# Kernel optimization log

Hardware: AMD Instinct MI355X
Metric: run time of the kernel (lower is better)

Reference implementation:

```python
import jax, jax.numpy as jnp
import numpy as np

N = 16384
F_IN = 256
F_OUT = 256


def setup_inputs() -> dict:
    key = jax.random.key(0)
    k1, k2, k3 = jax.random.split(key, 3)
    x = jax.random.normal(k1, (N, F_IN), dtype=jnp.float32)
    # dense 0/1 adjacency (original masks with adj[j] == 1)
    adj = jax.random.randint(k2, (N, N), 0, 2, dtype=jnp.int32)
    # glorot-uniform init for weight [2F_in, F_out]
    stdv = np.sqrt(6.0 / (2 * F_IN + F_OUT)).astype(np.float32)
    weight = jax.random.uniform(k3, (2 * F_IN, F_OUT), dtype=jnp.float32,
                                minval=-stdv, maxval=stdv)
    bias = jnp.zeros((F_OUT,), dtype=jnp.float32)
    return {"x": x, "adj": adj, "weight": weight, "bias": bias}


def reference(x, adj, weight, bias):
    # Mean over neighbors (adj row == 1): segment-mean expressed as a
    # normalized dense matmul -- equivalent to the per-row boolean-mask mean.
    a = adj.astype(x.dtype)                      # [N, N]
    deg = jnp.sum(a, axis=1, keepdims=True)      # [N, 1]
    x1 = (a @ x) / deg                           # [N, F] neighbor mean
    n_x = jnp.concatenate([x1, x], axis=1)       # [N, 2F]
    return n_x @ weight + bias                   # [N, F_out]
```

## Files before the change

### kernel.cpp

```cpp
#include <hip/hip_runtime.h>
#include <hip/hip_bf16.h>
#include <stdint.h>


typedef short bf16x8 __attribute__((ext_vector_type(8)));
typedef float f32x4  __attribute__((ext_vector_type(4)));

__device__ __forceinline__ uint32_t pack_bf16_rne(float lo, float hi) {
    uint32_t ul = __float_as_uint(lo);
    uint32_t uh = __float_as_uint(hi);
    ul = (ul + 0x7fffu + ((ul >> 16) & 1u)) >> 16;
    uh = (uh + 0x7fffu + ((uh >> 16) & 1u)) >> 16;
    return ul | (uh << 16);
}

__global__ __launch_bounds__(256) void k_transpose_w(const float* __restrict__ w,
                                                     uint16_t* __restrict__ wt) {
    int idx = blockIdx.x * 256 + threadIdx.x;
    int n = idx >> 8;
    int k = idx & 255;
    int row = (n < 256) ? k : (256 + k);
    int col = (n < 256) ? n : (n - 256);
    uint32_t u = __float_as_uint(w[row * 256 + col]);
    u = (u + 0x7fffu + ((u >> 16) & 1u)) >> 16;
    wt[idx] = (uint16_t)u;
}

__global__ __launch_bounds__(256) void k_small_gemm(const float* __restrict__ x,
                                                    const uint16_t* __restrict__ wt,
                                                    const float* __restrict__ bias,
                                                    uint16_t* __restrict__ yTt,
                                                    float* __restrict__ z) {
    __shared__ uint16_t As[128 * 32];
    __shared__ uint16_t Bs[128 * 32];

    const int t  = threadIdx.x;
    const int ct = blockIdx.x;
    const int rt = blockIdx.y;
    const int m0 = rt * 128;
    const int n0 = ct * 128;

    const int lane = t & 63, w = t >> 6;
    const int wr = w >> 1, wc = w & 1;
    const int l15 = lane & 15, quad = lane >> 4;

    f32x4 acc[4][4] = {};

    float4 a_reg[4];
    uint4  b_reg[2];

#pragma unroll
    for (int i = 0; i < 4; ++i) {
        int f4 = t + 256 * i, row = f4 >> 3, c4 = f4 & 7;
        a_reg[i] = *(const float4*)(x + (m0 + row) * 256 + c4 * 4);
    }
#pragma unroll
    for (int i = 0; i < 2; ++i) {
        int u4 = t + 256 * i, n_l = u4 >> 2, part = u4 & 3;
        b_reg[i] = *(const uint4*)(wt + (n0 + n_l) * 256 + part * 8);
    }

    for (int kk = 0; kk < 8; ++kk) {
        __syncthreads();
#pragma unroll
        for (int i = 0; i < 4; ++i) {
            int f4 = t + 256 * i, row = f4 >> 3, c4 = f4 & 7;
            uint2 p;
            p.x = pack_bf16_rne(a_reg[i].x, a_reg[i].y);
            p.y = pack_bf16_rne(a_reg[i].z, a_reg[i].w);
            *(uint2*)(As + row * 32 + c4 * 4) = p;
        }
#pragma unroll
        for (int i = 0; i < 2; ++i) {
            int u4 = t + 256 * i, n_l = u4 >> 2, part = u4 & 3;
            *(uint4*)(Bs + n_l * 32 + part * 8) = b_reg[i];
        }
        if (kk < 7) {
            int k0 = (kk + 1) * 32;
#pragma unroll
            for (int i = 0; i < 4; ++i) {
                int f4 = t + 256 * i, row = f4 >> 3, c4 = f4 & 7;
                a_reg[i] = *(const float4*)(x + (m0 + row) * 256 + k0 + c4 * 4);
            }
#pragma unroll
            for (int i = 0; i < 2; ++i) {
                int u4 = t + 256 * i, n_l = u4 >> 2, part = u4 & 3;
                b_reg[i] = *(const uint4*)(wt + (n0 + n_l) * 256 + k0 + part * 8);
            }
        }
        __syncthreads();

        bf16x8 a_frag[4], b_frag[4];
#pragma unroll
        for (int fr = 0; fr < 4; ++fr)
            a_frag[fr] = *(const bf16x8*)(As + (wr * 64 + fr * 16 + l15) * 32 + quad * 8);
#pragma unroll
        for (int fc = 0; fc < 4; ++fc)
            b_frag[fc] = *(const bf16x8*)(Bs + (wc * 64 + fc * 16 + l15) * 32 + quad * 8);
#pragma unroll
        for (int fr = 0; fr < 4; ++fr)
#pragma unroll
            for (int fc = 0; fc < 4; ++fc)
                acc[fr][fc] = __builtin_amdgcn_mfma_f32_16x16x32_bf16(
                    a_frag[fr], b_frag[fc], acc[fr][fc], 0, 0, 0);
    }

    if (ct < 2) {
#pragma unroll
        for (int fr = 0; fr < 4; ++fr) {
            int m_base = m0 + wr * 64 + fr * 16 + quad * 4;
#pragma unroll
            for (int fc = 0; fc < 4; ++fc) {
                int n_g = n0 + wc * 64 + fc * 16 + l15;
                uint2 pp;
                pp.x = pack_bf16_rne(acc[fr][fc][0], acc[fr][fc][1]);
                pp.y = pack_bf16_rne(acc[fr][fc][2], acc[fr][fc][3]);
                *(uint2*)(yTt + (size_t)(m_base >> 5) * 8192 + n_g * 32 + (m_base & 31)) = pp;
            }
        }
    } else {
#pragma unroll
        for (int fr = 0; fr < 4; ++fr) {
            int m_base = m0 + wr * 64 + fr * 16 + quad * 4;
#pragma unroll
            for (int fc = 0; fc < 4; ++fc) {
                int n_g = (n0 - 256) + wc * 64 + fc * 16 + l15;
                float bv = bias[n_g];
#pragma unroll
                for (int r = 0; r < 4; ++r)
                    z[(size_t)(m_base + r) * 256 + n_g] = acc[fr][fc][r] + bv;
            }
        }
    }
}

#define A_STRIDE 36
#define B_STRIDE 36
#define A_SZ (64 * A_STRIDE)
#define B_SZ (256 * B_STRIDE)
#define KITER 256

#define STEP(ARD, BRD, AWR, BWR, KK)                                            \
  do {                                                                          \
    if ((KK) < KITER - 2) {                                   \
      bN0 = *(const uint4*)(pB);                                                \
      bN1 = *(const uint4*)(pB + 4096);                                         \
      pB += 8192;                                                               \
    }                                                                           \
    if ((KK) < KITER - 3) {                                   \
      aN = pa4[0]; pa4 += 8;                                                    \
    }                                                                           \
    if ((KK) < KITER - 1) {                              \
      degp += aQ0.x + aQ0.y + aQ0.z + aQ0.w;                                    \
      uint2 pv;                                                                 \
      pv.x = (uint32_t)(aQ0.x | (aQ0.y << 16)) * 0x3F80u;                       \
      pv.y = (uint32_t)(aQ0.z | (aQ0.w << 16)) * 0x3F80u;                       \
      *(uint2*)&As##AWR[a_lds] = pv;                                            \
      *(uint4*)&Bs##BWR[b_lds0] = bC0;                                          \
      *(uint4*)&Bs##BWR[b_lds1] = bC1;                                          \
    }                                                                           \
    {                                                                           \
      bf16x8 af[2], bfr[4];                                                     \
      _Pragma("unroll") for (int fr = 0; fr < 2; ++fr) {                        \
        int row = wr * 32 + fr * 16 + l15;                                      \
        af[fr] = *(const bf16x8*)(As##ARD + row * A_STRIDE + quad * 8);         \
      }                                                                         \
      _Pragma("unroll") for (int fc = 0; fc < 4; ++fc) {                        \
        int n = wc * 64 + fc * 16 + l15;                                        \
        bfr[fc] = *(const bf16x8*)(Bs##BRD + n * B_STRIDE + quad * 8);          \
      }                                                                         \
      _Pragma("unroll") for (int fr = 0; fr < 2; ++fr)                          \
        _Pragma("unroll") for (int fc = 0; fc < 4; ++fc)                        \
          acc[fr][fc] = __builtin_amdgcn_mfma_f32_16x16x32_bf16(                \
              af[fr], bfr[fc], acc[fr][fc], 0, 0, 0);                           \
    }                                                                           \
    aQ0 = aQ1; aQ1 = aQ2; aQ2 = aN;                                             \
    bC0 = bN0; bC1 = bN1;                                                       \
    asm volatile("s_waitcnt lgkmcnt(0)\n\ts_barrier" ::: "memory");             \
  } while (0)

__global__ __launch_bounds__(512, 4) void k_big_gemm(const int* __restrict__ adj,
                                                     const uint16_t* __restrict__ yTt,
                                                     float* __restrict__ part,
                                                     int* __restrict__ degw) {
    __shared__ uint16_t As0[A_SZ], As1[A_SZ], As2[A_SZ];
    __shared__ uint16_t Bs0[B_SZ], Bs1[B_SZ], Bs2[B_SZ];

    const int t = threadIdx.x;
    const int m0 = blockIdx.x * 64;
    const int ky = blockIdx.y;
    const int lane = t & 63, w = t >> 6;
    const int wr = w >> 2, wc = w & 3;
    const int l15 = lane & 15, quad = lane >> 4;

    f32x4 acc[2][4] = {};

    const int a_n = t >> 3, a_c4 = t & 7;
    const int4* pa4 = (const int4*)(adj + (size_t)(m0 + a_n) * 16384 + ky * 8192) + a_c4;
    const int a_lds = a_n * A_STRIDE + a_c4 * 4;

    const uint16_t* pB = yTt + (size_t)(ky * 256) * 8192 + t * 8;
    const int b_s0 = t, b_s1 = t + 512;
    const int b_lds0 = (b_s0 >> 2) * B_STRIDE + (b_s0 & 3) * 8;
    const int b_lds1 = (b_s1 >> 2) * B_STRIDE + (b_s1 & 3) * 8;

    int4 a0 = pa4[0];
    int4 aQ0 = pa4[8];
    int4 aQ1 = pa4[16];
    int4 aQ2;
    int4 aN = aQ1;
    pa4 += 24;
    uint4 b00 = *(const uint4*)(pB);
    uint4 b01 = *(const uint4*)(pB + 4096);
    pB += 8192;
    uint4 bC0 = *(const uint4*)(pB);
    uint4 bC1 = *(const uint4*)(pB + 4096);
    pB += 8192;
    uint4 bN0 = bC0, bN1 = bC1;

    int degp = a0.x + a0.y + a0.z + a0.w;
    {
        uint2 pv;
        pv.x = (uint32_t)(a0.x | (a0.y << 16)) * 0x3F80u;
        pv.y = (uint32_t)(a0.z | (a0.w << 16)) * 0x3F80u;
        *(uint2*)&As0[a_lds] = pv;
        *(uint4*)&Bs0[b_lds0] = b00;
        *(uint4*)&Bs0[b_lds1] = b01;
    }
    asm volatile("s_waitcnt lgkmcnt(0)\n\ts_barrier" ::: "memory");

    for (int kk = 0; kk < KITER - 4; kk += 3) {
        STEP(0, 0, 1, 1, kk);
        STEP(1, 1, 2, 2, kk + 1);
        STEP(2, 2, 0, 0, kk + 2);
    }
    STEP(0, 0, 1, 1, 252);
    STEP(1, 1, 2, 2, 253);
    STEP(2, 2, 0, 0, 254);
    STEP(0, 0, 1, 1, 255);

    degp += __shfl_down(degp, 4);
    degp += __shfl_down(degp, 2);
    degp += __shfl_down(degp, 1);
    if ((t & 7) == 0) degw[ky * 16384 + m0 + a_n] = degp;

    float* pc = part + (size_t)ky * 16384 * 256;
#pragma unroll
    for (int fr = 0; fr < 2; ++fr) {
#pragma unroll
        for (int r = 0; r < 4; ++r) {
            int m_l = wr * 32 + fr * 16 + quad * 4 + r;
            size_t mrow = (size_t)(m0 + m_l) * 256;
#pragma unroll
            for (int fc = 0; fc < 4; ++fc) {
                int n_g = wc * 64 + fc * 16 + l15;
                pc[mrow + n_g] = acc[fr][fc][r];
            }
        }
    }
}

__global__ __launch_bounds__(256) void k_reduce(const float* __restrict__ part,
                                                const int* __restrict__ degw,
                                                const float* __restrict__ z,
                                                float* __restrict__ out) {
    int i4 = blockIdx.x * 256 + threadIdx.x;
    int m = i4 >> 6;
    float4 p0 = ((const float4*)part)[i4];
    float4 p1 = ((const float4*)part)[i4 + 16384 * 64];
    float4 zz = ((const float4*)z)[i4];
    float inv = 1.0f / (float)(degw[m] + degw[16384 + m]);
    float4 o;
    o.x = (p0.x + p1.x) * inv + zz.x;
    o.y = (p0.y + p1.y) * inv + zz.y;
    o.z = (p0.z + p1.z) * inv + zz.z;
    o.w = (p0.w + p1.w) * inv + zz.w;
    ((float4*)out)[i4] = o;
}

extern "C" void kernel_launch(void* const* d_in, const int* in_sizes, int n_in,
                              void* d_out, int out_size, void* d_ws, size_t ws_size,
                              hipStream_t stream) {
    const float* x      = (const float*)d_in[0];
    const int*   adj    = (const int*)d_in[1];
    const float* weight = (const float*)d_in[2];
    const float* bias   = (const float*)d_in[3];
    float* out = (float*)d_out;

    char* wsb = (char*)d_ws;
    uint16_t* wt   = (uint16_t*)(wsb);
    uint16_t* yTt  = (uint16_t*)(wsb + 262144);
    float*    z    = (float*)(wsb + 262144 + 8388608);
    float*    partb= (float*)(wsb + 262144 + 8388608 + 16777216);
    int*      degw = (int*)(wsb + 262144 + 8388608 + 16777216 + 33554432);

    k_transpose_w<<<512, 256, 0, stream>>>(weight, wt);
    k_small_gemm<<<dim3(4, 128), 256, 0, stream>>>(x, wt, bias, yTt, z);
    k_big_gemm<<<dim3(256, 2), 512, 0, stream>>>(adj, yTt, partb, degw);
    k_reduce<<<4096, 256, 0, stream>>>(partb, degw, z, out);
}
```

Before: 1.426 ms.

## Enlarge big GEMM tile to 128 rows with K=64 double-buffered register prefetch

Rewrites the adjacency GEMM kernel to use 128-row M tiles and 64-wide K steps, with each thread loading four int4 of adj and four uint4 of B per step. Global loads are issued two stages ahead into register sets and synchronised with explicit vmcnt waits, LDS goes from triple to double buffering, and MFMA sections run at raised wave priority. The larger tile halves how often each block re-reads B and doubles the MFMA work per barrier, at the cost of more registers and only 256 blocks, which means lower occupancy on the MI355X.

Result: slower. 1.664 ms (+16.7%).

```diff
diff --git a/kernel.cpp b/kernel.cpp
--- a/kernel.cpp
+++ b/kernel.cpp
@@ -134,123 +134,132 @@
     }
 }
 
-#define A_STRIDE 36
-#define B_STRIDE 36
-#define A_SZ (64 * A_STRIDE)
-#define B_SZ (256 * B_STRIDE)
-#define KITER 256
-
-#define STEP(ARD, BRD, AWR, BWR, KK)                                            \
-  do {                                                                          \
-    if ((KK) < KITER - 2) {                                   \
-      bN0 = *(const uint4*)(pB);                                                \
-      bN1 = *(const uint4*)(pB + 4096);                                         \
-      pB += 8192;                                                               \
-    }                                                                           \
-    if ((KK) < KITER - 3) {                                   \
-      aN = pa4[0]; pa4 += 8;                                                    \
-    }                                                                           \
-    if ((KK) < KITER - 1) {                              \
-      degp += aQ0.x + aQ0.y + aQ0.z + aQ0.w;                                    \
-      uint2 pv;                                                                 \
-      pv.x = (uint32_t)(aQ0.x | (aQ0.y << 16)) * 0x3F80u;                       \
-      pv.y = (uint32_t)(aQ0.z | (aQ0.w << 16)) * 0x3F80u;                       \
-      *(uint2*)&As##AWR[a_lds] = pv;                                            \
-      *(uint4*)&Bs##BWR[b_lds0] = bC0;                                          \
-      *(uint4*)&Bs##BWR[b_lds1] = bC1;                                          \
-    }                                                                           \
-    {                                                                           \
-      bf16x8 af[2], bfr[4];                                                     \
-      _Pragma("unroll") for (int fr = 0; fr < 2; ++fr) {                        \
-        int row = wr * 32 + fr * 16 + l15;                                      \
-        af[fr] = *(const bf16x8*)(As##ARD + row * A_STRIDE + quad * 8);         \
-      }                                                                         \
-      _Pragma("unroll") for (int fc = 0; fc < 4; ++fc) {                        \
-        int n = wc * 64 + fc * 16 + l15;                                        \
-        bfr[fc] = *(const bf16x8*)(Bs##BRD + n * B_STRIDE + quad * 8);          \
-      }                                                                         \
-      _Pragma("unroll") for (int fr = 0; fr < 2; ++fr)                          \
-        _Pragma("unroll") for (int fc = 0; fc < 4; ++fc)                        \
-          acc[fr][fc] = __builtin_amdgcn_mfma_f32_16x16x32_bf16(                \
-              af[fr], bfr[fc], acc[fr][fc], 0, 0, 0);                           \
-    }                                                                           \
-    aQ0 = aQ1; aQ1 = aQ2; aQ2 = aN;                                             \
-    bC0 = bN0; bC1 = bN1;                                                       \
-    asm volatile("s_waitcnt lgkmcnt(0)\n\ts_barrier" ::: "memory");             \
+#define BM 128
+#define NT 128
+#define A_ST 72
+#define B_ST 72
+
+#define ISSUE(SET, STEP_)                                                     \
+  do {                                                                        \
+    const int4*  ap_ = pa4 + (size_t)(STEP_) * 16;                            \
+    const uint4* bp_ = pb4 + (size_t)(STEP_) * 2048;                          \
+    aR[SET][0] = ap_[0]; aR[SET][1] = ap_[1];                                 \
+    aR[SET][2] = ap_[2]; aR[SET][3] = ap_[3];                                 \
+    bR[SET][0] = bp_[0]; bR[SET][1] = bp_[1];                                 \
+    bR[SET][2] = bp_[2]; bR[SET][3] = bp_[3];                                 \
   } while (0)
 
-__global__ __launch_bounds__(512, 4) void k_big_gemm(const int* __restrict__ adj,
-                                                     const uint16_t* __restrict__ yTt,
-                                                     float* __restrict__ part,
-                                                     int* __restrict__ degw) {
-    __shared__ uint16_t As0[A_SZ], As1[A_SZ], As2[A_SZ];
-    __shared__ uint16_t Bs0[B_SZ], Bs1[B_SZ], Bs2[B_SZ];
+#define STAGE(SET, BUF)                                                       \
+  do {                                                                        \
+    degp += aR[SET][0].x + aR[SET][0].y + aR[SET][0].z + aR[SET][0].w         \
+          + aR[SET][1].x + aR[SET][1].y + aR[SET][1].z + aR[SET][1].w         \
+          + aR[SET][2].x + aR[SET][2].y + aR[SET][2].z + aR[SET][2].w         \
+          + aR[SET][3].x + aR[SET][3].y + aR[SET][3].z + aR[SET][3].w;        \
+    uint4 w0_, w1_;                                                           \
+    w0_.x = (uint32_t)(aR[SET][0].x | (aR[SET][0].y << 16)) * 0x3F80u;        \
+    w0_.y = (uint32_t)(aR[SET][0].z | (aR[SET][0].w << 16)) * 0x3F80u;        \
+    w0_.z = (uint32_t)(aR[SET][1].x | (aR[SET][1].y << 16)) * 0x3F80u;        \
+    w0_.w = (uint32_t)(aR[SET][1].z | (aR[SET][1].w << 16)) * 0x3F80u;        \
+    w1_.x = (uint32_t)(aR[SET][2].x | (aR[SET][2].y << 16)) * 0x3F80u;        \
+    w1_.y = (uint32_t)(aR[SET][2].z | (aR[SET][2].w << 16)) * 0x3F80u;        \
+    w1_.z = (uint32_t)(aR[SET][3].x | (aR[SET][3].y << 16)) * 0x3F80u;        \
+    w1_.w = (uint32_t)(aR[SET][3].z | (aR[SET][3].w << 16)) * 0x3F80u;        \
+    *(uint4*)&As[BUF][a_wr]      = w0_;                                       \
+    *(uint4*)&As[BUF][a_wr + 8]  = w1_;                                       \
+    *(uint4*)&Bs[BUF][b_wr]      = bR[SET][0];                                \
+    *(uint4*)&Bs[BUF][b_wr + 8]  = bR[SET][1];                                \
+    *(uint4*)&Bs[BUF][b_wr + 16] = bR[SET][2];                                \
+    *(uint4*)&Bs[BUF][b_wr + 24] = bR[SET][3];                                \
+  } while (0)
+
+#define COMPUTE(BUF)                                                          \
+  do {                                                                        \
+    _Pragma("unroll") for (int kh = 0; kh < 2; ++kh) {                        \
+      bf16x8 af[4], bfr[4];                                                   \
+      _Pragma("unroll") for (int fr = 0; fr < 4; ++fr)                        \
+        af[fr] = *(const bf16x8*)&As[BUF][(wr * 64 + fr * 16 + l15) * A_ST +  \
+                                          kh * 32 + quad * 8];                \
+      _Pragma("unroll") for (int fc = 0; fc < 4; ++fc)                        \
+        bfr[fc] = *(const bf16x8*)&Bs[BUF][(wc * 64 + fc * 16 + l15) * B_ST + \
+                                           kh * 32 + quad * 8];               \
+      _Pragma("unroll") for (int fr = 0; fr < 4; ++fr)                        \
+        _Pragma("unroll") for (int fc = 0; fc < 4; ++fc)                      \
+          acc[fr][fc] = __builtin_amdgcn_mfma_f32_16x16x32_bf16(              \
+              af[fr], bfr[fc], acc[fr][fc], 0, 0, 0);                         \
+    }                                                                         \
+  } while (0)
+
+__global__ __launch_bounds__(512) void k_big_gemm(const int* __restrict__ adj,
+                                                  const uint16_t* __restrict__ yTt,
+                                                  float* __restrict__ part,
+                                                  int* __restrict__ degw) {
+    __shared__ __align__(16) uint16_t As[2][BM * A_ST];
+    __shared__ __align__(16) uint16_t Bs[2][256 * B_ST];
 
     const int t = threadIdx.x;
-    const int m0 = blockIdx.x * 64;
+    const int m0 = blockIdx.x * BM;
     const int ky = blockIdx.y;
     const int lane = t & 63, w = t >> 6;
     const int wr = w >> 2, wc = w & 3;
     const int l15 = lane & 15, quad = lane >> 4;
 
-    f32x4 acc[2][4] = {};
-
-    const int a_n = t >> 3, a_c4 = t & 7;
-    const int4* pa4 = (const int4*)(adj + (size_t)(m0 + a_n) * 16384 + ky * 8192) + a_c4;
-    const int a_lds = a_n * A_STRIDE + a_c4 * 4;
-
-    const uint16_t* pB = yTt + (size_t)(ky * 256) * 8192 + t * 8;
-    const int b_s0 = t, b_s1 = t + 512;
-    const int b_lds0 = (b_s0 >> 2) * B_STRIDE + (b_s0 & 3) * 8;
-    const int b_lds1 = (b_s1 >> 2) * B_STRIDE + (b_s1 & 3) * 8;
-
-    int4 a0 = pa4[0];
-    int4 aQ0 = pa4[8];
-    int4 aQ1 = pa4[16];
-    int4 aQ2;
-    int4 aN = aQ1;
-    pa4 += 24;
-    uint4 b00 = *(const uint4*)(pB);
-    uint4 b01 = *(const uint4*)(pB + 4096);
-    pB += 8192;
-    uint4 bC0 = *(const uint4*)(pB);
-    uint4 bC1 = *(const uint4*)(pB + 4096);
-    pB += 8192;
-    uint4 bN0 = bC0, bN1 = bC1;
-
-    int degp = a0.x + a0.y + a0.z + a0.w;
-    {
-        uint2 pv;
-        pv.x = (uint32_t)(a0.x | (a0.y << 16)) * 0x3F80u;
-        pv.y = (uint32_t)(a0.z | (a0.w << 16)) * 0x3F80u;
-        *(uint2*)&As0[a_lds] = pv;
-        *(uint4*)&Bs0[b_lds0] = b00;
-        *(uint4*)&Bs0[b_lds1] = b01;
-    }
+    f32x4 acc[4][4] = {};
+
+    const int a_row = t >> 2, a_c = t & 3;
+    const int4* pa4 = (const int4*)(adj + (size_t)(m0 + a_row) * 16384 + ky * 8192) + a_c * 4;
+    const int a_wr = a_row * A_ST + a_c * 16;
+
+    const int b_kt = t >> 8, b_n = t & 255;
+    const uint4* pb4 = (const uint4*)(yTt + ((size_t)ky * 256 + b_kt) * 8192 + b_n * 32);
+    const int b_wr = b_n * B_ST + b_kt * 32;
+
+    int4  aR[2][4];
+    uint4 bR[2][4];
+    int degp = 0;
+
+    ISSUE(0, 0);
+    asm volatile("" ::: "memory");
+    ISSUE(1, 1);
+    asm volatile("s_waitcnt vmcnt(8)" ::: "memory");
+    STAGE(0, 0);
     asm volatile("s_waitcnt lgkmcnt(0)\n\ts_barrier" ::: "memory");
 
-    for (int kk = 0; kk < KITER - 4; kk += 3) {
-        STEP(0, 0, 1, 1, kk);
-        STEP(1, 1, 2, 2, kk + 1);
-        STEP(2, 2, 0, 0, kk + 2);
-    }
-    STEP(0, 0, 1, 1, 252);
-    STEP(1, 1, 2, 2, 253);
-    STEP(2, 2, 0, 0, 254);
-    STEP(0, 0, 1, 1, 255);
-
-    degp += __shfl_down(degp, 4);
+    for (int tt = 0; tt < NT - 2; tt += 2) {
+        ISSUE(0, tt + 2);
+        asm volatile("s_waitcnt vmcnt(8)" ::: "memory");
+        STAGE(1, 1);
+        __builtin_amdgcn_s_setprio(1);
+        COMPUTE(0);
+        __builtin_amdgcn_s_setprio(0);
+        asm volatile("s_waitcnt lgkmcnt(0)\n\ts_barrier" ::: "memory");
+
+        ISSUE(1, tt + 3);
+        asm volatile("s_waitcnt vmcnt(8)" ::: "memory");
+        STAGE(0, 0);
+        __builtin_amdgcn_s_setprio(1);
+        COMPUTE(1);
+        __builtin_amdgcn_s_setprio(0);
+        asm volatile("s_waitcnt lgkmcnt(0)\n\ts_barrier" ::: "memory");
+    }
+    asm volatile("s_waitcnt vmcnt(0)" ::: "memory");
+    STAGE(1, 1);
+    __builtin_amdgcn_s_setprio(1);
+    COMPUTE(0);
+    __builtin_amdgcn_s_setprio(0);
+    asm volatile("s_waitcnt lgkmcnt(0)\n\ts_barrier" ::: "memory");
+    COMPUTE(1);
+
     degp += __shfl_down(degp, 2);
     degp += __shfl_down(degp, 1);
-    if ((t & 7) == 0) degw[ky * 16384 + m0 + a_n] = degp;
-
-    float* pc = part + (size_t)ky * 16384 * 256;
-#pragma unroll
-    for (int fr = 0; fr < 2; ++fr) {
+    if ((t & 3) == 0) degw[ky * 16384 + m0 + a_row] = degp;
+
+    float* pc = part + (size_t)ky * 16384 * 256 + (size_t)m0 * 256;
+#pragma unroll
+    for (int fr = 0; fr < 4; ++fr) {
 #pragma unroll
         for (int r = 0; r < 4; ++r) {
-            int m_l = wr * 32 + fr * 16 + quad * 4 + r;
-            size_t mrow = (size_t)(m0 + m_l) * 256;
+            int m_l = wr * 64 + fr * 16 + quad * 4 + r;
+            size_t mrow = (size_t)m_l * 256;
 #pragma unroll
             for (int fc = 0; fc < 4; ++fc) {
                 int n_g = wc * 64 + fc * 16 + l15;
@@ -296,6 +305,6 @@
 
     k_transpose_w<<<512, 256, 0, stream>>>(weight, wt);
     k_small_gemm<<<dim3(4, 128), 256, 0, stream>>>(x, wt, bias, yTt, z);
-    k_big_gemm<<<dim3(256, 2), 512, 0, stream>>>(adj, yTt, partb, degw);
+    k_big_gemm<<<dim3(128, 2), 512, 0, stream>>>(adj, yTt, partb, degw);
     k_reduce<<<4096, 256, 0, stream>>>(partb, degw, z, out);
 }
```

## Load B fragments directly from global into registers and remap blocks per XCD

Applied to the files above, without the earlier changes.

Removes the LDS staging for the B operand (the transposed y matrix). Each wave now loads its MFMA B fragments straight from global memory into registers, prefetched one step ahead, which drops the LDS writes and reads and shrinks shared memory to the A buffers only. The block index is also remapped so that blocks with the same K-half and neighbouring M tiles land on the same XCD, aiming for better L2 reuse of adjacency rows and B. In exchange, B tiles that were shared through LDS are now fetched redundantly by each wave row, raising global/L2 traffic and register pressure.

Result: slower. 1.494 ms (+4.8%).

```diff
diff --git a/kernel.cpp b/kernel.cpp
--- a/kernel.cpp
+++ b/kernel.cpp
@@ -135,47 +135,39 @@
 }
 
 #define A_STRIDE 36
-#define B_STRIDE 36
 #define A_SZ (64 * A_STRIDE)
-#define B_SZ (256 * B_STRIDE)
 #define KITER 256
 
-#define STEP(ARD, BRD, AWR, BWR, KK)                                            \
+#define STEP(ARD, AWR, KK)                                                      \
   do {                                                                          \
-    if ((KK) < KITER - 2) {                                   \
-      bN0 = *(const uint4*)(pB);                                                \
-      bN1 = *(const uint4*)(pB + 4096);                                         \
+    if ((KK) < KITER - 1) {                                \
+      _Pragma("unroll") for (int fc = 0; fc < 4; ++fc)                          \
+        bN[fc] = *(const bf16x8*)(pB + fc * 512);                               \
       pB += 8192;                                                               \
     }                                                                           \
     if ((KK) < KITER - 3) {                                   \
       aN = pa4[0]; pa4 += 8;                                                    \
     }                                                                           \
-    if ((KK) < KITER - 1) {                              \
+    if ((KK) < KITER - 1) {                           \
       degp += aQ0.x + aQ0.y + aQ0.z + aQ0.w;                                    \
       uint2 pv;                                                                 \
       pv.x = (uint32_t)(aQ0.x | (aQ0.y << 16)) * 0x3F80u;                       \
       pv.y = (uint32_t)(aQ0.z | (aQ0.w << 16)) * 0x3F80u;                       \
       *(uint2*)&As##AWR[a_lds] = pv;                                            \
-      *(uint4*)&Bs##BWR[b_lds0] = bC0;                                          \
-      *(uint4*)&Bs##BWR[b_lds1] = bC1;                                          \
     }                                                                           \
     {                                                                           \
-      bf16x8 af[2], bfr[4];                                                     \
+      bf16x8 af[2];                                                             \
       _Pragma("unroll") for (int fr = 0; fr < 2; ++fr) {                        \
         int row = wr * 32 + fr * 16 + l15;                                      \
         af[fr] = *(const bf16x8*)(As##ARD + row * A_STRIDE + quad * 8);         \
       }                                                                         \
-      _Pragma("unroll") for (int fc = 0; fc < 4; ++fc) {                        \
-        int n = wc * 64 + fc * 16 + l15;                                        \
-        bfr[fc] = *(const bf16x8*)(Bs##BRD + n * B_STRIDE + quad * 8);          \
-      }                                                                         \
       _Pragma("unroll") for (int fr = 0; fr < 2; ++fr)                          \
         _Pragma("unroll") for (int fc = 0; fc < 4; ++fc)                        \
           acc[fr][fc] = __builtin_amdgcn_mfma_f32_16x16x32_bf16(                \
-              af[fr], bfr[fc], acc[fr][fc], 0, 0, 0);                           \
+              af[fr], bC[fc], acc[fr][fc], 0, 0, 0);                            \
     }                                                                           \
     aQ0 = aQ1; aQ1 = aQ2; aQ2 = aN;                                             \
-    bC0 = bN0; bC1 = bN1;                                                       \
+    _Pragma("unroll") for (int fc = 0; fc < 4; ++fc) bC[fc] = bN[fc];           \
     asm volatile("s_waitcnt lgkmcnt(0)\n\ts_barrier" ::: "memory");             \
   } while (0)
 
@@ -184,11 +176,12 @@
                                                      float* __restrict__ part,
                                                      int* __restrict__ degw) {
     __shared__ uint16_t As0[A_SZ], As1[A_SZ], As2[A_SZ];
-    __shared__ uint16_t Bs0[B_SZ], Bs1[B_SZ], Bs2[B_SZ];
 
     const int t = threadIdx.x;
-    const int m0 = blockIdx.x * 64;
-    const int ky = blockIdx.y;
+    const int id   = blockIdx.x + (int)gridDim.x * blockIdx.y;
+    const int xcd  = id & 7, slot = id >> 3;
+    const int ky   = xcd >> 2;
+    const int m0   = ((xcd & 3) * 64 + slot) * 64;
     const int lane = t & 63, w = t >> 6;
     const int wr = w >> 2, wc = w & 3;
     const int l15 = lane & 15, quad = lane >> 4;
@@ -199,45 +192,43 @@
     const int4* pa4 = (const int4*)(adj + (size_t)(m0 + a_n) * 16384 + ky * 8192) + a_c4;
     const int a_lds = a_n * A_STRIDE + a_c4 * 4;
 
-    const uint16_t* pB = yTt + (size_t)(ky * 256) * 8192 + t * 8;
-    const int b_s0 = t, b_s1 = t + 512;
-    const int b_lds0 = (b_s0 >> 2) * B_STRIDE + (b_s0 & 3) * 8;
-    const int b_lds1 = (b_s1 >> 2) * B_STRIDE + (b_s1 & 3) * 8;
+    const uint16_t* pB = yTt + (size_t)(ky * 256) * 8192
+                       + (size_t)(wc * 64 + l15) * 32 + quad * 8;
+
+    bf16x8 bC[4], bN[4];
+    int4 aQ0, aQ1, aQ2, aN;
+    int degp;
 
     int4 a0 = pa4[0];
-    int4 aQ0 = pa4[8];
-    int4 aQ1 = pa4[16];
-    int4 aQ2;
-    int4 aN = aQ1;
+    aQ0 = pa4[8];
+    aQ1 = pa4[16];
+    aQ2 = aQ1;
+    aN  = aQ1;
     pa4 += 24;
-    uint4 b00 = *(const uint4*)(pB);
-    uint4 b01 = *(const uint4*)(pB + 4096);
+#pragma unroll
+    for (int fc = 0; fc < 4; ++fc) bN[fc] = *(const bf16x8*)(pB + fc * 512);
     pB += 8192;
-    uint4 bC0 = *(const uint4*)(pB);
-    uint4 bC1 = *(const uint4*)(pB + 4096);
-    pB += 8192;
-    uint4 bN0 = bC0, bN1 = bC1;
-
-    int degp = a0.x + a0.y + a0.z + a0.w;
+#pragma unroll
+    for (int fc = 0; fc < 4; ++fc) bC[fc] = bN[fc];
+
+    degp = a0.x + a0.y + a0.z + a0.w;
     {
         uint2 pv;
         pv.x = (uint32_t)(a0.x | (a0.y << 16)) * 0x3F80u;
         pv.y = (uint32_t)(a0.z | (a0.w << 16)) * 0x3F80u;
         *(uint2*)&As0[a_lds] = pv;
-        *(uint4*)&Bs0[b_lds0] = b00;
-        *(uint4*)&Bs0[b_lds1] = b01;
     }
     asm volatile("s_waitcnt lgkmcnt(0)\n\ts_barrier" ::: "memory");
 
     for (int kk = 0; kk < KITER - 4; kk += 3) {
-        STEP(0, 0, 1, 1, kk);
-        STEP(1, 1, 2, 2, kk + 1);
-        STEP(2, 2, 0, 0, kk + 2);
-    }
-    STEP(0, 0, 1, 1, 252);
-    STEP(1, 1, 2, 2, 253);
-    STEP(2, 2, 0, 0, 254);
-    STEP(0, 0, 1, 1, 255);
+        STEP(0, 1, kk);
+        STEP(1, 2, kk + 1);
+        STEP(2, 0, kk + 2);
+    }
+    STEP(0, 1, 252);
+    STEP(1, 2, 253);
+    STEP(2, 0, 254);
+    STEP(0, 1, 255);
 
     degp += __shfl_down(degp, 4);
     degp += __shfl_down(degp, 2);
```

## Deepen adjacency prefetch, use nontemporal loads/stores, remap blocks across XCDs

Applied to the files above, without the earlier changes.

Reads the streamed adjacency matrix with nontemporal loads and deepens its register prefetch queue from three to four stages to hide more global latency. Writes partial results with nontemporal stores so they do not pollute cache. Remaps the flat block id so that each XCD handles one K-half and a contiguous row range, so the shared B operand (yTt) stays local to each XCD's L2. Costs extra registers for the deeper queue, which could hurt occupancy at 512 threads with 4 blocks per CU.

New measurement: 1.425 ms. No clear change (-0.0%).

```diff
diff --git a/kernel.cpp b/kernel.cpp
--- a/kernel.cpp
+++ b/kernel.cpp
@@ -5,6 +5,7 @@
 
 typedef short bf16x8 __attribute__((ext_vector_type(8)));
 typedef float f32x4  __attribute__((ext_vector_type(4)));
+typedef int   i32x4  __attribute__((ext_vector_type(4)));
 
 __device__ __forceinline__ uint32_t pack_bf16_rne(float lo, float hi) {
     uint32_t ul = __float_as_uint(lo);
@@ -147,14 +148,14 @@
       bN1 = *(const uint4*)(pB + 4096);                                         \
       pB += 8192;                                                               \
     }                                                                           \
-    if ((KK) < KITER - 3) {                                   \
-      aN = pa4[0]; pa4 += 8;                                                    \
+    if ((KK) < KITER - 4) {                     \
+      aN = __builtin_nontemporal_load(pa4); pa4 += 8;                           \
     }                                                                           \
     if ((KK) < KITER - 1) {                              \
-      degp += aQ0.x + aQ0.y + aQ0.z + aQ0.w;                                    \
+      degp += q1.x + q1.y + q1.z + q1.w;                                        \
       uint2 pv;                                                                 \
-      pv.x = (uint32_t)(aQ0.x | (aQ0.y << 16)) * 0x3F80u;                       \
-      pv.y = (uint32_t)(aQ0.z | (aQ0.w << 16)) * 0x3F80u;                       \
+      pv.x = (uint32_t)(q1.x | (q1.y << 16)) * 0x3F80u;                         \
+      pv.y = (uint32_t)(q1.z | (q1.w << 16)) * 0x3F80u;                         \
       *(uint2*)&As##AWR[a_lds] = pv;                                            \
       *(uint4*)&Bs##BWR[b_lds0] = bC0;                                          \
       *(uint4*)&Bs##BWR[b_lds1] = bC1;                                          \
@@ -174,7 +175,7 @@
           acc[fr][fc] = __builtin_amdgcn_mfma_f32_16x16x32_bf16(                \
               af[fr], bfr[fc], acc[fr][fc], 0, 0, 0);                           \
     }                                                                           \
-    aQ0 = aQ1; aQ1 = aQ2; aQ2 = aN;                                             \
+    q1 = q2; q2 = q3; q3 = aN;                                                  \
     bC0 = bN0; bC1 = bN1;                                                       \
     asm volatile("s_waitcnt lgkmcnt(0)\n\ts_barrier" ::: "memory");             \
   } while (0)
@@ -187,8 +188,10 @@
     __shared__ uint16_t Bs0[B_SZ], Bs1[B_SZ], Bs2[B_SZ];
 
     const int t = threadIdx.x;
-    const int m0 = blockIdx.x * 64;
-    const int ky = blockIdx.y;
+    const int id   = blockIdx.x + (int)gridDim.x * blockIdx.y;
+    const int xcd  = id & 7, slot = id >> 3;
+    const int ky   = xcd >> 2;
+    const int m0   = ((xcd & 3) * 64 + slot) * 64;
     const int lane = t & 63, w = t >> 6;
     const int wr = w >> 2, wc = w & 3;
     const int l15 = lane & 15, quad = lane >> 4;
@@ -196,7 +199,7 @@
     f32x4 acc[2][4] = {};
 
     const int a_n = t >> 3, a_c4 = t & 7;
-    const int4* pa4 = (const int4*)(adj + (size_t)(m0 + a_n) * 16384 + ky * 8192) + a_c4;
+    const i32x4* pa4 = (const i32x4*)(adj + (size_t)(m0 + a_n) * 16384 + ky * 8192) + a_c4;
     const int a_lds = a_n * A_STRIDE + a_c4 * 4;
 
     const uint16_t* pB = yTt + (size_t)(ky * 256) * 8192 + t * 8;
@@ -204,12 +207,12 @@
     const int b_lds0 = (b_s0 >> 2) * B_STRIDE + (b_s0 & 3) * 8;
     const int b_lds1 = (b_s1 >> 2) * B_STRIDE + (b_s1 & 3) * 8;
 
-    int4 a0 = pa4[0];
-    int4 aQ0 = pa4[8];
-    int4 aQ1 = pa4[16];
-    int4 aQ2;
-    int4 aN = aQ1;
-    pa4 += 24;
+    i32x4 a0 = __builtin_nontemporal_load(pa4);
+    i32x4 q1 = __builtin_nontemporal_load(pa4 + 8);
+    i32x4 q2 = __builtin_nontemporal_load(pa4 + 16);
+    i32x4 q3 = __builtin_nontemporal_load(pa4 + 24);
+    i32x4 aN = q3;
+    pa4 += 32;
     uint4 b00 = *(const uint4*)(pB);
     uint4 b01 = *(const uint4*)(pB + 4096);
     pB += 8192;
@@ -254,7 +257,7 @@
 #pragma unroll
             for (int fc = 0; fc < 4; ++fc) {
                 int n_g = wc * 64 + fc * 16 + l15;
-                pc[mrow + n_g] = acc[fr][fc][r];
+                __builtin_nontemporal_store(acc[fr][fc][r], &pc[mrow + n_g]);
             }
         }
     }
```
